# Optimization experiments

Hardware: AMD Instinct MI355X
Metric: run time of the kernel (lower is better)

Reference implementation:

```python
import jax, jax.numpy as jnp
import numpy as np

TEMPERATURE = 0.5
EPS = 1e-10

N, C, H, W = 8, 256, 96, 96
T, V = 32, 256
NUM_CLASSES = 19


def setup_inputs() -> dict:
    key = jax.random.key(0)
    k1, k2, k3, k4 = jax.random.split(key, 4)
    features = jax.random.normal(k1, (N, C, H, W), dtype=jnp.float32)
    batch_inds = jax.random.randint(k2, (T,), 0, N, dtype=jnp.int32)
    sample_inds = jax.random.randint(k3, (T, V), 0, H * W).astype(jnp.int64)
    labels = jax.random.randint(k4, (T,), 0, NUM_CLASSES, dtype=jnp.int32)
    return {"features": features, "batch_inds": batch_inds,
            "sample_inds": sample_inds, "labels": labels}


def reference(features, batch_inds, sample_inds, labels):
    n, c, h, w = features.shape
    t, v = sample_inds.shape
    # --- anchor sampling: gather V pixels per (image, class) pair ---
    f = features.reshape(n, c, h * w)            # (N, C, HW)
    g = f[batch_inds]                            # (T, C, HW)
    sampled = jnp.take_along_axis(g, sample_inds[:, None, :], axis=2)  # (T, C, V)
    # --- contrastive loss ---
    norm = jnp.maximum(jnp.linalg.norm(sampled, axis=1, keepdims=True), 1e-12)
    feats = sampled / norm                       # L2 normalize along C
    feats = jnp.swapaxes(feats, 1, 2).reshape(t * v, c)  # (T*V, C)
    lab = jnp.repeat(labels, v)                  # (T*V,)
    dot = (feats @ feats.T) / TEMPERATURE        # (T*V, T*V)
    eq = (lab[:, None] == lab[None, :]).astype(dot.dtype)
    diag = jnp.eye(t * v, dtype=dot.dtype)
    pos_mask = eq * (1.0 - diag)
    neg_mask = 1.0 - eq
    # stable SupCon loss: logsumexp over {self-exp + all negatives}
    logits = dot - jax.lax.stop_gradient(jnp.max(dot, axis=1, keepdims=True))
    exp_logits = jnp.exp(logits)
    neg_sum = jnp.sum(exp_logits * neg_mask, axis=1, keepdims=True)
    log_prob = logits - jnp.log(exp_logits + neg_sum)
    mean_log_prob_pos = jnp.sum(pos_mask * log_prob, axis=1) / jnp.maximum(
        jnp.sum(pos_mask, axis=1), EPS)
    return -jnp.mean(mean_log_prob_pos)
```

## Files before the change

### kernel.cpp

```cpp
#include <hip/hip_runtime.h>
#include <hip/hip_bf16.h>


namespace {

constexpr int kC = 256;
constexpr int kHW = 96 * 96;
constexpr int kT = 32;
constexpr int kV = 256;
constexpr int kM = kT * kV;

typedef __attribute__((ext_vector_type(8))) short short8;
typedef __attribute__((ext_vector_type(4))) float f32x4;

__device__ inline unsigned short f2bf(float x) {
  __hip_bfloat16 h = __float2bfloat16(x);
  return __builtin_bit_cast(unsigned short, h);
}
__device__ inline float bf2f(unsigned short u) {
  unsigned int v = ((unsigned int)u) << 16;
  return __builtin_bit_cast(float, v);
}
__device__ inline float exp_2am2(float a) {
  return exp2f(fmaf(a, 2.8853900818f, -2.8853900818f));
}
__device__ inline void load_lds16(const unsigned short* g, unsigned short* l) {
  __builtin_amdgcn_global_load_lds(
      (const __attribute__((address_space(1))) void*)g,
      (__attribute__((address_space(3))) void*)l, 16, 0, 0);
}


__device__ inline void stage_ct(const unsigned short* __restrict__ F2,
                                unsigned short* lds, int g0, int tid) {
#pragma unroll
  for (int i = 0; i < 2; ++i) {
    const int nslot = i * 512 + tid;
    load_lds16(F2 + (((size_t)g0 * 8) << 9) + ((size_t)nslot << 3),
               lds + ((size_t)nslot << 3));
  }
}
__device__ inline void stage_a(const unsigned short* __restrict__ F2,
                               unsigned short* lds, int g0, int tid) {
#pragma unroll
  for (int i = 0; i < 4; ++i) {
    const int nslot = i * 512 + tid;
    load_lds16(F2 + (((size_t)g0 * 8) << 9) + ((size_t)nslot << 3),
               lds + ((size_t)nslot << 3));
  }
}

}

__global__ __launch_bounds__(256) void k_prep(
    const int* __restrict__ labels, float* __restrict__ ns,
    float* __restrict__ out, int out_size, int* __restrict__ nact,
    ushort2* __restrict__ list, float* __restrict__ cscale,
    int* __restrict__ nneg, ushort2* __restrict__ neglist) {
  const int tid = (int)threadIdx.x;
  const int b = (int)blockIdx.x;
  for (int i = b * 256 + tid; i < kM; i += 64 * 256) ns[i] = 0.f;
  if (b != 0) return;
  __shared__ int s_lab[kT];
  if (tid < kT) s_lab[tid] = labels[tid];
  if (tid == 0) {
    *nact = 0;
    *nneg = 0;
  }
  for (int i = tid; i < out_size; i += 256) out[i] = 0.f;
  __syncthreads();
  if (tid < kT) {
    int m = 0;
    for (int u = 0; u < kT; ++u) m += (s_lab[u] == s_lab[tid]) ? 1 : 0;
    cscale[tid] = 1.f / ((float)(m * kV - 1) * (float)kM);
  }
  for (int p = tid; p < kT * kT; p += 256) {
    const int ti = p >> 5, tj = p & 31;
    if (s_lab[ti] == s_lab[tj]) {
      int base = atomicAdd(nact, 64);
#pragma unroll
      for (int a = 0; a < 8; ++a)
#pragma unroll
        for (int bb = 0; bb < 8; ++bb) {
          ushort2 e;
          e.x = (unsigned short)(ti * 8 + a);
          e.y = (unsigned short)(tj * 8 + bb);
          list[base + a * 8 + bb] = e;
        }
    } else if (ti < tj) {
      int idx = atomicAdd(nneg, 1);
      ushort2 e;
      e.x = (unsigned short)ti;
      e.y = (unsigned short)tj;
      neglist[idx] = e;
    }
  }
}

__global__ __launch_bounds__(256) void k_gather(
    const float* __restrict__ feat, const int* __restrict__ binds,
    const int* __restrict__ sinds, unsigned short* __restrict__ FT) {
  const int b = (int)blockIdx.x;
  const int c = (int)blockIdx.y;
  __shared__ alignas(16) float row[kHW];
  __shared__ int s_match[kT + 1];
  if (threadIdx.x == 0) {
    int cnt = 0;
    for (int t = 0; t < kT; ++t)
      if (binds[t] == b) s_match[1 + cnt++] = t;
    s_match[0] = cnt;
  }
  __syncthreads();
  const int cnt = s_match[0];
  if (cnt == 0) return;
  const float4* src4 = (const float4*)(feat + ((size_t)b * kC + c) * kHW);
  for (int i = (int)threadIdx.x; i < kHW / 4; i += 256)
    ((float4*)row)[i] = src4[i];
  __syncthreads();
  unsigned short* dst = FT + (size_t)c * kM;
  for (int mi = 1; mi <= cnt; ++mi) {
    const int t = s_match[mi];
    const int p = sinds[t * kV + threadIdx.x];
    dst[t * kV + threadIdx.x] = f2bf(row[p]);
  }
}

__global__ __launch_bounds__(256) void k_norm(
    const unsigned short* __restrict__ FT, unsigned short* __restrict__ F2) {
  constexpr int PAD = 40;
  const int v0 = (int)blockIdx.x * 32;
  __shared__ alignas(16) unsigned short tile[kC][PAD];
  __shared__ float part[8][32];
  __shared__ float s_inv[32];
  const int tid = (int)threadIdx.x;
  {
    const int p4 = tid & 3, cb = tid >> 2;
    for (int c = cb; c < kC; c += 64) {
      int4 d = *(const int4*)(FT + (size_t)c * kM + v0 + p4 * 8);
      *(int4*)&tile[c][p4 * 8] = d;
    }
  }
  __syncthreads();
  {
    const int v = tid & 31, oct = tid >> 5;
    float ss = 0.f;
    for (int c = oct * 32; c < oct * 32 + 32; ++c) {
      float x = bf2f(tile[c][v]);
      ss += x * x;
    }
    part[oct][v] = ss;
  }
  __syncthreads();
  if (tid < 32) {
    float ss = 0.f;
#pragma unroll
    for (int o = 0; o < 8; ++o) ss += part[o][tid];
    s_inv[tid] = 1.0f / fmaxf(sqrtf(ss), 1e-12f);
  }
  __syncthreads();
#pragma unroll
  for (int p = 0; p < 4; ++p) {
    const int slot = p * 256 + tid;
    const int l16s = slot & 15;
    const int qs = (slot >> 4) & 3;
    const int kss = (slot >> 6) & 7;
    const int gl = slot >> 9;
    const int vloc = gl * 16 + l16s;
    const int c0 = kss * 32 + qs * 8;
    const float inv = s_inv[vloc];
    alignas(16) unsigned short o[8];
#pragma unroll
    for (int k = 0; k < 8; ++k) o[k] = f2bf(bf2f(tile[c0 + k][vloc]) * inv);
    *(int4*)(F2 + ((size_t)(((v0 >> 4) + gl) * 8 + kss) << 9) +
             ((qs * 16 + l16s) << 3)) = *(const int4*)o;
  }
}

__global__ __launch_bounds__(512, 2) void k_neg(
    const unsigned short* __restrict__ F2, const int* __restrict__ nneg,
    const ushort2* __restrict__ neglist, float* __restrict__ ns) {
  const int tid = (int)threadIdx.x;
  const int w = tid >> 6, lane = tid & 63, q = lane >> 4, l16 = lane & 15;
  __shared__ alignas(16) unsigned short Bt[2][8192];
  __shared__ float colacc[256];
  const int n = *nneg;
  const int laneofs = (q * 16 + l16) << 3;

  for (int job = (int)blockIdx.x; job < n; job += (int)gridDim.x) {
    const ushort2 e = neglist[job];
    const int ti = e.x, tj = e.y;
    if (tid < 256) colacc[tid] = 0.f;

    short8 af[2][8];
#pragma unroll 1
    for (int p = 0; p < 4; ++p) {
      stage_a(F2, &Bt[0][0], ti * 16 + p * 4, tid);
      __syncthreads();
      if ((w >> 1) == p) {
        const int lg = (w & 1) * 2;
#pragma unroll
        for (int rg = 0; rg < 2; ++rg)
#pragma unroll
          for (int ks = 0; ks < 8; ++ks)
            af[rg][ks] = *(const short8*)(
                &Bt[0][0] + ((size_t)((lg + rg) * 8 + ks) << 9) + laneofs);
      }
      __syncthreads();
    }

    stage_ct(F2, &Bt[0][0], tj * 16, tid);
    float rowacc[2][4] = {};
    int cur = 0;
#pragma unroll 1
    for (int ct = 0; ct < 8; ++ct) {
      __syncthreads();
      if (ct < 7) stage_ct(F2, &Bt[cur ^ 1][0], tj * 16 + (ct + 1) * 2, tid);
      const unsigned short* bbase = &Bt[cur][0] + laneofs;
      f32x4 a00 = {0.f, 0.f, 0.f, 0.f}, a01 = a00, a10 = a00, a11 = a00;
#pragma unroll
      for (int ks = 0; ks < 8; ++ks) {
        short8 b0 = *(const short8*)(bbase + ((size_t)ks << 9));
        short8 b1 = *(const short8*)(bbase + ((size_t)(8 + ks) << 9));
        a00 = __builtin_amdgcn_mfma_f32_16x16x32_bf16(af[0][ks], b0, a00,
                                                      0, 0, 0);
        a01 = __builtin_amdgcn_mfma_f32_16x16x32_bf16(af[0][ks], b1, a01,
                                                      0, 0, 0);
        a10 = __builtin_amdgcn_mfma_f32_16x16x32_bf16(af[1][ks], b0, a10,
                                                      0, 0, 0);
        a11 = __builtin_amdgcn_mfma_f32_16x16x32_bf16(af[1][ks], b1, a11,
                                                      0, 0, 0);
      }
      float col0 = 0.f, col1 = 0.f;
#pragma unroll
      for (int r = 0; r < 4; ++r) {
        float e00 = exp_2am2(a00[r]), e01 = exp_2am2(a01[r]);
        float e10 = exp_2am2(a10[r]), e11 = exp_2am2(a11[r]);
        rowacc[0][r] += e00 + e01;
        rowacc[1][r] += e10 + e11;
        col0 += e00 + e10;
        col1 += e01 + e11;
      }
      col0 += __shfl_xor(col0, 16, 64);
      col0 += __shfl_xor(col0, 32, 64);
      col1 += __shfl_xor(col1, 16, 64);
      col1 += __shfl_xor(col1, 32, 64);
      if (q == 0) {
        atomicAdd(&colacc[ct * 32 + l16], col0);
        atomicAdd(&colacc[ct * 32 + 16 + l16], col1);
      }
      cur ^= 1;
    }
    __syncthreads();
    if (tid < 256) atomicAdd(&ns[tj * 256 + tid], colacc[tid]);
#pragma unroll
    for (int rg = 0; rg < 2; ++rg)
#pragma unroll
      for (int r = 0; r < 4; ++r) {
        float v = rowacc[rg][r];
        v += __shfl_xor(v, 1, 64);
        v += __shfl_xor(v, 2, 64);
        v += __shfl_xor(v, 4, 64);
        v += __shfl_xor(v, 8, 64);
        if (l16 == 0)
          atomicAdd(&ns[ti * 256 + w * 32 + rg * 16 + q * 4 + r], v);
      }
    __syncthreads();
  }
}

__global__ __launch_bounds__(256, 2) void k_pos(
    const unsigned short* __restrict__ F2, const float* __restrict__ ns,
    const int* __restrict__ nact, const ushort2* __restrict__ list,
    const float* __restrict__ cscale, float* __restrict__ out) {
  const int tid = (int)threadIdx.x;
  const int w = tid >> 6, lane = tid & 63, q = lane >> 4, l16 = lane & 15;
  __shared__ float s_pos[4];
  const int n = *nact;
  const unsigned short* lanep = F2 + ((q * 16 + l16) << 3);

  float pos = 0.f;
  for (int idx = (int)blockIdx.x * 4 + w; idx < n;
       idx += (int)gridDim.x * 4) {
    const ushort2 e = list[idx];
    const int r32 = e.x, c32 = e.y;
    const int ga = r32 * 2, gb = c32 * 2;
    short8 af[2][8], bf[2][8];
#pragma unroll
    for (int rg = 0; rg < 2; ++rg)
#pragma unroll
      for (int ks = 0; ks < 8; ++ks) {
        af[rg][ks] =
            *(const short8*)(lanep + ((size_t)((ga + rg) * 8 + ks) << 9));
        bf[rg][ks] =
            *(const short8*)(lanep + ((size_t)((gb + rg) * 8 + ks) << 9));
      }
    float nsv[2][4];
#pragma unroll
    for (int rg = 0; rg < 2; ++rg)
#pragma unroll
      for (int r = 0; r < 4; ++r)
        nsv[rg][r] = ns[r32 * 32 + rg * 16 + q * 4 + r];
    const float scale = cscale[r32 >> 3];

    f32x4 a00 = {0.f, 0.f, 0.f, 0.f}, a01 = a00, a10 = a00, a11 = a00;
#pragma unroll
    for (int ks = 0; ks < 8; ++ks) {
      a00 = __builtin_amdgcn_mfma_f32_16x16x32_bf16(af[0][ks], bf[0][ks], a00,
                                                    0, 0, 0);
      a01 = __builtin_amdgcn_mfma_f32_16x16x32_bf16(af[0][ks], bf[1][ks], a01,
                                                    0, 0, 0);
      a10 = __builtin_amdgcn_mfma_f32_16x16x32_bf16(af[1][ks], bf[0][ks], a10,
                                                    0, 0, 0);
      a11 = __builtin_amdgcn_mfma_f32_16x16x32_bf16(af[1][ks], bf[1][ks], a11,
                                                    0, 0, 0);
    }
    float tpos = 0.f;
#pragma unroll
    for (int rg = 0; rg < 2; ++rg)
#pragma unroll
      for (int cg = 0; cg < 2; ++cg) {
        const f32x4 acc =
            (rg == 0) ? (cg == 0 ? a00 : a01) : (cg == 0 ? a10 : a11);
        const int jc = c32 * 32 + cg * 16 + l16;
#pragma unroll
        for (int r = 0; r < 4; ++r) {
          const int i = r32 * 32 + rg * 16 + q * 4 + r;
          if (i != jc) {
            float d = fmaf(acc[r], 2.f, -2.f);
            tpos += d - __logf(exp_2am2(acc[r]) + nsv[rg][r]);
          }
        }
      }
    pos += scale * tpos;
  }

#pragma unroll
  for (int m = 1; m < 64; m <<= 1) pos += __shfl_xor(pos, m, 64);
  if (lane == 0) s_pos[w] = pos;
  __syncthreads();
  if (tid == 0)
    atomicAdd(out, -(s_pos[0] + s_pos[1] + s_pos[2] + s_pos[3]));
}

extern "C" void kernel_launch(void* const* d_in, const int* in_sizes, int n_in,
                              void* d_out, int out_size, void* d_ws,
                              size_t ws_size, hipStream_t stream) {
  const float* feat = (const float*)d_in[0];
  const int* binds = (const int*)d_in[1];
  const int* sinds = (const int*)d_in[2];
  const int* labels = (const int*)d_in[3];
  float* out = (float*)d_out;
  unsigned short* FT = (unsigned short*)d_ws;
  unsigned short* F2 = FT + (size_t)kC * kM;
  float* ns = (float*)(F2 + (size_t)kM * kC);
  int* nact = (int*)(ns + kM);
  float* cscale = (float*)(nact + 8);
  ushort2* list = (ushort2*)(cscale + 32);
  int* nneg = (int*)(list + 65536);
  ushort2* neglist = (ushort2*)(nneg + 8);

  k_prep<<<64, 256, 0, stream>>>(labels, ns, out, out_size, nact, list,
                                 cscale, nneg, neglist);
  k_gather<<<dim3(8, kC), 256, 0, stream>>>(feat, binds, sinds, FT);
  k_norm<<<kM / 32, 256, 0, stream>>>(FT, F2);
  k_neg<<<512, 512, 0, stream>>>(F2, nneg, neglist, ns);
  k_pos<<<512, 256, 0, stream>>>(F2, ns, nact, list, cscale, out);
}
```

Baseline: 165.3 us.

## Exploit dot-product symmetry to halve positive-pair MFMA tile work

The positive-pair work list now holds only upper-triangular 32x32 tiles. Off-diagonal tiles are flagged with a mirror bit so one matrix product gives both the row-side and column-side loss terms, each with its own negative-sum and class scale. This is meant to cut the MFMA and operand loads in the positive pass roughly in half. The cost is an extra logf per element and a few more loads for mirrored tiles.

```diff
diff --git a/kernel.cpp b/kernel.cpp
--- a/kernel.cpp
+++ b/kernel.cpp
@@ -77,16 +77,33 @@
   for (int p = tid; p < kT * kT; p += 256) {
     const int ti = p >> 5, tj = p & 31;
     if (s_lab[ti] == s_lab[tj]) {
-      int base = atomicAdd(nact, 64);
-#pragma unroll
-      for (int a = 0; a < 8; ++a)
-#pragma unroll
-        for (int bb = 0; bb < 8; ++bb) {
-          ushort2 e;
-          e.x = (unsigned short)(ti * 8 + a);
-          e.y = (unsigned short)(tj * 8 + bb);
-          list[base + a * 8 + bb] = e;
+      if (ti < tj) {
+        int base = atomicAdd(nact, 64);
+#pragma unroll
+        for (int a = 0; a < 8; ++a)
+#pragma unroll
+          for (int bb = 0; bb < 8; ++bb) {
+            ushort2 e;
+            e.x = (unsigned short)(ti * 8 + a);
+            e.y = (unsigned short)((tj * 8 + bb) | 0x8000);
+            list[base + a * 8 + bb] = e;
+          }
+      } else if (ti == tj) {
+        int base = atomicAdd(nact, 36);
+        int k = 0;
+        for (int a = 0; a < 8; ++a) {
+          ushort2 d;
+          d.x = (unsigned short)(ti * 8 + a);
+          d.y = (unsigned short)(ti * 8 + a);
+          list[base + k++] = d;
+          for (int bb = a + 1; bb < 8; ++bb) {
+            ushort2 e;
+            e.x = (unsigned short)(ti * 8 + a);
+            e.y = (unsigned short)((ti * 8 + bb) | 0x8000);
+            list[base + k++] = e;
+          }
         }
+      }
     } else if (ti < tj) {
       int idx = atomicAdd(nneg, 1);
       ushort2 e;
@@ -282,7 +299,9 @@
   for (int idx = (int)blockIdx.x * 4 + w; idx < n;
        idx += (int)gridDim.x * 4) {
     const ushort2 e = list[idx];
-    const int r32 = e.x, c32 = e.y;
+    const int r32 = e.x;
+    const int c32 = e.y & 0x7fff;
+    const bool mirror = (e.y & 0x8000) != 0;
     const int ga = r32 * 2, gb = c32 * 2;
     short8 af[2][8], bf[2][8];
 #pragma unroll
@@ -300,7 +319,11 @@
 #pragma unroll
       for (int r = 0; r < 4; ++r)
         nsv[rg][r] = ns[r32 * 32 + rg * 16 + q * 4 + r];
-    const float scale = cscale[r32 >> 3];
+    float nsc[2];
+    nsc[0] = ns[c32 * 32 + l16];
+    nsc[1] = ns[c32 * 32 + 16 + l16];
+    const float scr = cscale[r32 >> 3];
+    const float scc = cscale[c32 >> 3];
 
     f32x4 a00 = {0.f, 0.f, 0.f, 0.f}, a01 = a00, a10 = a00, a11 = a00;
 #pragma unroll
@@ -314,24 +337,29 @@
       a11 = __builtin_amdgcn_mfma_f32_16x16x32_bf16(af[1][ks], bf[1][ks], a11,
                                                     0, 0, 0);
     }
-    float tpos = 0.f;
+    float tr = 0.f, tc = 0.f;
 #pragma unroll
     for (int rg = 0; rg < 2; ++rg)
 #pragma unroll
       for (int cg = 0; cg < 2; ++cg) {
         const f32x4 acc =
             (rg == 0) ? (cg == 0 ? a00 : a01) : (cg == 0 ? a10 : a11);
-        const int jc = c32 * 32 + cg * 16 + l16;
 #pragma unroll
         for (int r = 0; r < 4; ++r) {
-          const int i = r32 * 32 + rg * 16 + q * 4 + r;
-          if (i != jc) {
-            float d = fmaf(acc[r], 2.f, -2.f);
-            tpos += d - __logf(exp_2am2(acc[r]) + nsv[rg][r]);
+          const float d = fmaf(acc[r], 2.f, -2.f);
+          const float ee = exp_2am2(acc[r]);
+          if (mirror) {
+            tr += d - __logf(ee + nsv[rg][r]);
+            tc += d - __logf(ee + nsc[cg]);
+          } else {
+            const int i = r32 * 32 + rg * 16 + q * 4 + r;
+            const int jc = c32 * 32 + cg * 16 + l16;
+            if (i != jc) tr += d - __logf(ee + nsv[rg][r]);
           }
         }
       }
-    pos += scale * tpos;
+    pos += scr * tr;
+    if (mirror) pos += scc * tc;
   }
 
 #pragma unroll
```

After: 163.2 us. No clear change (-1.3%).
